# Kernel optimization log

Measured on AMD Instinct MI355X. Metric: run time of the kernel, lower is better.

Reference implementation:

```python
import jax, jax.numpy as jnp
import numpy as np

N, E, B = 100000, 3200000, 512
D_IN, D_H, HID = 500, 64, 200
NUM_CLASSES = 80
EPS_BN = 1e-5


def _sage(x, src, dst, Wl, bl, Wr):
    # PyG SAGEConv (mean aggr): out = lin_l(mean_{j->i} x_j) + lin_r(x_i)
    n = x.shape[0]
    agg = jax.ops.segment_sum(x[src], dst, num_segments=n)          # [n, d_in]
    deg = jax.ops.segment_sum(jnp.ones((src.shape[0],), x.dtype), dst, num_segments=n)
    mean = agg / jnp.maximum(deg, 1.0)[:, None]
    return mean @ Wl + bl + x @ Wr


def _bn(c, g, b):
    # BatchNorm1d, training-mode batch statistics (biased var)
    mu = c.mean(0)
    var = c.var(0)
    return (c - mu) / jnp.sqrt(var + EPS_BN) * g + b


def setup_inputs() -> dict:
    key = jax.random.key(0)
    ks = jax.random.split(key, 16)
    p = lambda k, shape: jax.random.normal(k, shape, dtype=jnp.float32) * 0.05
    z = lambda d: jnp.zeros((d,), jnp.float32)
    o = lambda d: jnp.ones((d,), jnp.float32)
    return {
        "x": jax.random.uniform(ks[0], (N, D_IN), dtype=jnp.float32),
        "edge_index": jax.random.randint(ks[1], (2, E), 0, N),
        "batch": jnp.sort(jax.random.randint(ks[2], (N,), 0, B)),
        "y": jax.random.randint(ks[3], (B,), 0, NUM_CLASSES),
        "conv1_Wl": p(ks[4], (D_IN, D_H)), "conv1_bl": z(D_H), "conv1_Wr": p(ks[5], (D_IN, D_H)),
        "conv2_Wl": p(ks[6], (D_H, D_H)),  "conv2_bl": z(D_H), "conv2_Wr": p(ks[7], (D_H, D_H)),
        "conv3_Wl": p(ks[8], (D_H, D_H)),  "conv3_bl": z(D_H), "conv3_Wr": p(ks[9], (D_H, D_H)),
        "lin1_W": p(ks[10], (D_H, HID)), "lin1_b": z(HID),
        "bn1_g": o(HID), "bn1_beta": z(HID),
        "lin2_W": p(ks[11], (HID, HID // 2)), "lin2_b": z(HID // 2),
        "bn2_g": o(HID // 2), "bn2_beta": z(HID // 2),
        "lin3_W": p(ks[12], (HID // 2, HID // 2)), "lin3_b": z(HID // 2),
        "bn3_g": o(HID // 2), "bn3_beta": z(HID // 2),
        "lin4_W": p(ks[13], (HID // 2, NUM_CLASSES)), "lin4_b": z(NUM_CLASSES),
    }


def reference(x, edge_index, batch, y,
              conv1_Wl, conv1_bl, conv1_Wr,
              conv2_Wl, conv2_bl, conv2_Wr,
              conv3_Wl, conv3_bl, conv3_Wr,
              lin1_W, lin1_b, bn1_g, bn1_beta,
              lin2_W, lin2_b, bn2_g, bn2_beta,
              lin3_W, lin3_b, bn3_g, bn3_beta,
              lin4_W, lin4_b):
    src, dst = edge_index[0], edge_index[1]
    # F.normalize(x, p=1.0, dim=-1)
    xn = x / jnp.maximum(jnp.abs(x).sum(-1, keepdims=True), 1e-12)
    e = _sage(xn, src, dst, conv1_Wl, conv1_bl, conv1_Wr)
    e = _sage(e, src, dst, conv2_Wl, conv2_bl, conv2_Wr)
    e = _sage(e, src, dst, conv3_Wl, conv3_bl, conv3_Wr)
    # global_mean_pool over graph ids
    sums = jax.ops.segment_sum(e, batch, num_segments=B)             # [B, 64]
    cnts = jax.ops.segment_sum(jnp.ones((e.shape[0],), e.dtype), batch, num_segments=B)
    c = sums / jnp.maximum(cnts, 1.0)[:, None]
    # dropout (p=0.1) omitted for a deterministic reference
    c = c @ lin1_W + lin1_b
    b = jnp.tanh(_bn(c, bn1_g, bn1_beta))
    c = b @ lin2_W + lin2_b
    b = jnp.tanh(_bn(c, bn2_g, bn2_beta))
    c = b @ lin3_W + lin3_b
    b = jnp.tanh(_bn(c, bn3_g, bn3_beta))
    return b @ lin4_W + lin4_b                                       # [B, 80]
```

## Files before the change

kernel.cpp:

```cpp
#include <hip/hip_runtime.h>
#include <hip/hip_bf16.h>

#define NN 100000
#define NE 3200000
#define NB 512
#define DIN 500
#define DH 64
#define HIDN 200
#define NCLS 80

#define NBUK 256
#define NPB 391
#define EPB 16384
#define NBLK_E ((NE + EPB - 1) / EPB)

typedef __attribute__((ext_vector_type(8))) short bf16x8;
typedef __attribute__((ext_vector_type(4))) float f32x4;

__device__ __forceinline__ short f2bf(float f) {
    union { float f; unsigned u; } v; v.f = f;
    unsigned r = v.u + 0x7FFF + ((v.u >> 16) & 1);
    return (short)(r >> 16);
}
__device__ __forceinline__ float bf2f(short s) {
    union { unsigned u; float f; } v; v.u = ((unsigned)(unsigned short)s) << 16;
    return v.f;
}

__global__ void bukhist_kernel(const int* __restrict__ dst, int* __restrict__ block_hist) {
    __shared__ int h[NBUK];
    for (int i = threadIdx.x; i < NBUK; i += 256) h[i] = 0;
    __syncthreads();
    int base = blockIdx.x * EPB;
    int end = min(base + EPB, NE);
    for (int e = base + threadIdx.x; e < end; e += 256)
        atomicAdd(&h[dst[e] / NPB], 1);
    __syncthreads();
    for (int i = threadIdx.x; i < NBUK; i += 256)
        block_hist[blockIdx.x * NBUK + i] = h[i];
}

__global__ void bukoff_kernel(int* __restrict__ block_hist, int* __restrict__ buk_base) {
    __shared__ int tot[NBUK];
    __shared__ int sc[NBUK];
    int b = threadIdx.x;
    int s = 0;
    for (int i = 0; i < NBLK_E; ++i) s += block_hist[i * NBUK + b];
    tot[b] = s; sc[b] = s;
    __syncthreads();
    for (int o = 1; o < NBUK; o <<= 1) {
        int t = (b >= o) ? sc[b - o] : 0;
        __syncthreads();
        sc[b] += t;
        __syncthreads();
    }
    int excl = sc[b] - tot[b];
    buk_base[b] = excl;
    if (b == NBUK - 1) buk_base[NBUK] = excl + tot[b];
    int run = excl;
    for (int i = 0; i < NBLK_E; ++i) {
        int idx = i * NBUK + b;
        int v = block_hist[idx];
        block_hist[idx] = run;
        run += v;
    }
}

__global__ void bukscat_kernel(const int* __restrict__ src, const int* __restrict__ dst,
                               const int* __restrict__ block_hist, int* __restrict__ bpack) {
    __shared__ int cur[NBUK];
    for (int i = threadIdx.x; i < NBUK; i += 256)
        cur[i] = block_hist[blockIdx.x * NBUK + i];
    __syncthreads();
    int base = blockIdx.x * EPB;
    int end = min(base + EPB, NE);
    for (int e = base + threadIdx.x; e < end; e += 256) {
        int d = dst[e];
        int bk = d / NPB;
        int p = atomicAdd(&cur[bk], 1);
        bpack[p] = (src[e] << 9) | (d - bk * NPB);
    }
}

__global__ void bukfin_kernel(const int* __restrict__ buk_base, const int* __restrict__ bpack,
                              int* __restrict__ row_ptr, float* __restrict__ invdeg,
                              int* __restrict__ csr_src) {
    __shared__ int cnt[NPB];
    __shared__ int cbase[NPB];
    int bk = blockIdx.x;
    int n0 = bk * NPB;
    int nloc = min(n0 + NPB, NN) - n0;
    for (int i = threadIdx.x; i < nloc; i += 256) cnt[i] = 0;
    __syncthreads();
    int beg = buk_base[bk], end = buk_base[bk + 1];
    for (int p = beg + threadIdx.x; p < end; p += 256)
        atomicAdd(&cnt[bpack[p] & 511], 1);
    __syncthreads();
    if (threadIdx.x == 0) {
        int run = beg;
        for (int i = 0; i < nloc; ++i) { int v = cnt[i]; cbase[i] = run; run += v; }
    }
    __syncthreads();
    for (int i = threadIdx.x; i < nloc; i += 256) {
        row_ptr[n0 + i] = cbase[i];
        invdeg[n0 + i] = 1.0f / fmaxf((float)cnt[i], 1.0f);
        cnt[i] = cbase[i];
    }
    if (bk == NBUK - 1 && threadIdx.x == 0) row_ptr[NN] = end;
    __syncthreads();
    for (int p = beg + threadIdx.x; p < end; p += 256) {
        int v = bpack[p];
        int q = atomicAdd(&cnt[v & 511], 1);
        csr_src[q] = v >> 9;
    }
}

__global__ void wprep_kernel(const float* __restrict__ Wl, const float* __restrict__ Wr,
                             short* __restrict__ Wb, int K, int KP) {
    int id = blockIdx.x * blockDim.x + threadIdx.x;
    if (id >= 128 * KP) return;
    int col = id / KP, k = id - col * KP;
    float v = 0.f;
    if (k < K) v = (col < 64) ? Wl[(size_t)k * 64 + col] : Wr[(size_t)k * 64 + (col - 64)];
    Wb[(size_t)col * KP + k] = f2bf(v);
}

__launch_bounds__(256)
__global__ void gemm_direct(const float* __restrict__ in, const short* __restrict__ Wb,
                            short* __restrict__ Hl, float* __restrict__ Hr) {
    const int tid = threadIdx.x;
    const int w = tid >> 6, l = tid & 63;
    const int q = l >> 4, r16 = l & 15;
    const int tile0 = blockIdx.x * 64 + w * 16;
    const int arow_i = tile0 + r16;
    const bool ok = arow_i < NN;
    const float* arow = in + (size_t)(ok ? arow_i : 0) * DIN + q * 8;

    f32x4 acc[8];
#pragma unroll
    for (int c = 0; c < 8; ++c) acc[c] = (f32x4){0.f, 0.f, 0.f, 0.f};
    float pabs = 0.f;

#pragma unroll
    for (int t = 0; t < 16; ++t) {
        float v[8];
        if (t < 15) {
            const float4 f0 = *(const float4*)(arow + t * 32);
            const float4 f1 = *(const float4*)(arow + t * 32 + 4);
            v[0] = f0.x; v[1] = f0.y; v[2] = f0.z; v[3] = f0.w;
            v[4] = f1.x; v[5] = f1.y; v[6] = f1.z; v[7] = f1.w;
        } else {
#pragma unroll
            for (int i = 0; i < 8; ++i) {
                int gk = t * 32 + q * 8 + i;
                v[i] = (gk < DIN) ? arow[t * 32 + i] : 0.f;
            }
        }
        short sh[8];
#pragma unroll
        for (int i = 0; i < 8; ++i) { pabs += fabsf(v[i]); sh[i] = f2bf(v[i]); }
        bf16x8 a = *(bf16x8*)sh;
#pragma unroll
        for (int c = 0; c < 8; ++c) {
            bf16x8 b = *(const bf16x8*)(Wb + (size_t)(c * 16 + r16) * 512 + t * 32 + q * 8);
            acc[c] = __builtin_amdgcn_mfma_f32_16x16x32_bf16(a, b, acc[c], 0, 0, 0);
        }
    }

    pabs += __shfl_xor(pabs, 16, 64);
    pabs += __shfl_xor(pabs, 32, 64);
    float sval = 1.0f / fmaxf(pabs, 1e-12f);

#pragma unroll
    for (int rr = 0; rr < 4; ++rr) {
        int lrow = q * 4 + rr;
        float srow = __shfl(sval, lrow, 64);
        int grow = tile0 + lrow;
        if (grow < NN) {
#pragma unroll
            for (int c = 0; c < 8; ++c) {
                float o = acc[c][rr] * srow;
                if (c < 4) Hl[(size_t)grow * 64 + c * 16 + r16] = f2bf(o);
                else       Hr[(size_t)grow * 64 + (c - 4) * 16 + r16] = o;
            }
        }
    }
}

__launch_bounds__(256)
__global__ void gemm64_mfma(const short* __restrict__ ein, const short* __restrict__ Wb,
                            short* __restrict__ Hl, float* __restrict__ Hr) {
    const int tid = threadIdx.x;
    const int row0 = blockIdx.x * 64;
    const int w = tid >> 6, l = tid & 63;
    const int q = l >> 4, r16 = l & 15;
    const int arow = row0 + w * 16 + r16;
    const bool ok = arow < NN;
    const short* ap = ein + (size_t)(ok ? arow : 0) * 64 + q * 8;
    f32x4 acc[8];
#pragma unroll
    for (int c = 0; c < 8; ++c) acc[c] = (f32x4){0.f, 0.f, 0.f, 0.f};
    const bf16x8 z8 = (bf16x8){0, 0, 0, 0, 0, 0, 0, 0};
#pragma unroll
    for (int t = 0; t < 2; ++t) {
        bf16x8 a = ok ? *(const bf16x8*)(ap + t * 32) : z8;
#pragma unroll
        for (int c = 0; c < 8; ++c) {
            bf16x8 b = *(const bf16x8*)(Wb + (size_t)(c * 16 + r16) * 64 + t * 32 + q * 8);
            acc[c] = __builtin_amdgcn_mfma_f32_16x16x32_bf16(a, b, acc[c], 0, 0, 0);
        }
    }
#pragma unroll
    for (int c = 0; c < 8; ++c) {
#pragma unroll
        for (int rr = 0; rr < 4; ++rr) {
            int grow = row0 + w * 16 + q * 4 + rr;
            if (grow < NN) {
                if (c < 4) Hl[(size_t)grow * 64 + c * 16 + r16] = f2bf(acc[c][rr]);
                else       Hr[(size_t)grow * 64 + (c - 4) * 16 + r16] = acc[c][rr];
            }
        }
    }
}

template<bool LAST>
__launch_bounds__(256, 8)
__global__ void gather_kernel(const int* __restrict__ row_ptr, const int* __restrict__ csr_src,
                              const short* __restrict__ Hl, const float* __restrict__ Hr,
                              const float* __restrict__ invdeg, const float* __restrict__ bl,
                              short* __restrict__ ebf, float* __restrict__ ef32) {
    int node = blockIdx.x * 4 + (threadIdx.x >> 6);
    if (node >= NN) return;
    int lane = threadIdx.x & 63;
    int ng = lane >> 3;
    int fl = lane & 7;
    int beg = row_ptr[node], end = row_ptr[node + 1];
    float a0[8], a1[8];
#pragma unroll
    for (int j = 0; j < 8; ++j) { a0[j] = 0.f; a1[j] = 0.f; }
    int p = beg + ng;
    for (; p + 24 < end; p += 32) {
        int s0 = csr_src[p];
        int s1 = csr_src[p + 8];
        int s2 = csr_src[p + 16];
        int s3 = csr_src[p + 24];
        bf16x8 v0 = *(const bf16x8*)(Hl + (size_t)s0 * 64 + fl * 8);
        bf16x8 v1 = *(const bf16x8*)(Hl + (size_t)s1 * 64 + fl * 8);
        bf16x8 v2 = *(const bf16x8*)(Hl + (size_t)s2 * 64 + fl * 8);
        bf16x8 v3 = *(const bf16x8*)(Hl + (size_t)s3 * 64 + fl * 8);
#pragma unroll
        for (int j = 0; j < 8; ++j) {
            a0[j] += bf2f(v0[j]) + bf2f(v2[j]);
            a1[j] += bf2f(v1[j]) + bf2f(v3[j]);
        }
    }
    for (; p < end; p += 8) {
        int s0 = csr_src[p];
        bf16x8 v0 = *(const bf16x8*)(Hl + (size_t)s0 * 64 + fl * 8);
#pragma unroll
        for (int j = 0; j < 8; ++j) a0[j] += bf2f(v0[j]);
    }
#pragma unroll
    for (int j = 0; j < 8; ++j) a0[j] += a1[j];
#pragma unroll
    for (int m = 8; m < 64; m <<= 1)
#pragma unroll
        for (int j = 0; j < 8; ++j) a0[j] += __shfl_xor(a0[j], m, 64);
    if (ng == 0) {
        float idg = invdeg[node];
        const float4 h0 = *(const float4*)(Hr + (size_t)node * 64 + fl * 8);
        const float4 h1 = *(const float4*)(Hr + (size_t)node * 64 + fl * 8 + 4);
        float o[8];
        o[0] = a0[0] * idg + bl[fl * 8 + 0] + h0.x;
        o[1] = a0[1] * idg + bl[fl * 8 + 1] + h0.y;
        o[2] = a0[2] * idg + bl[fl * 8 + 2] + h0.z;
        o[3] = a0[3] * idg + bl[fl * 8 + 3] + h0.w;
        o[4] = a0[4] * idg + bl[fl * 8 + 4] + h1.x;
        o[5] = a0[5] * idg + bl[fl * 8 + 5] + h1.y;
        o[6] = a0[6] * idg + bl[fl * 8 + 6] + h1.z;
        o[7] = a0[7] * idg + bl[fl * 8 + 7] + h1.w;
        if (LAST) {
            *(float4*)(ef32 + (size_t)node * 64 + fl * 8)     = make_float4(o[0], o[1], o[2], o[3]);
            *(float4*)(ef32 + (size_t)node * 64 + fl * 8 + 4) = make_float4(o[4], o[5], o[6], o[7]);
        } else {
            short s[8];
#pragma unroll
            for (int j = 0; j < 8; ++j) s[j] = f2bf(o[j]);
            *(bf16x8*)(ebf + (size_t)node * 64 + fl * 8) = *(bf16x8*)s;
        }
    }
}

__global__ void gseg_kernel(const int* __restrict__ batch, int* __restrict__ gstart) {
    int i = blockIdx.x * blockDim.x + threadIdx.x;
    if (i >= NN) return;
    int bc = batch[i];
    int bp = (i == 0) ? -1 : batch[i - 1];
    for (int b = bp + 1; b <= bc; ++b) gstart[b] = i;
    if (i == NN - 1)
        for (int b = bc + 1; b <= NB; ++b) gstart[b] = NN;
}

__launch_bounds__(256)
__global__ void pool_seg(const float* __restrict__ e, const int* __restrict__ gstart,
                         float* __restrict__ c0) {
    __shared__ float part[4][64];
    int b = blockIdx.x;
    int w = threadIdx.x >> 6, lane = threadIdx.x & 63;
    int s = gstart[b], t = gstart[b + 1];
    float acc = 0.f;
    for (int i = s + w; i < t; i += 4) acc += e[(size_t)i * 64 + lane];
    part[w][lane] = acc;
    __syncthreads();
    if (w == 0) {
        float v = part[0][lane] + part[1][lane] + part[2][lane] + part[3][lane];
        c0[b * 64 + lane] = v / fmaxf((float)(t - s), 1.0f);
    }
}

__global__ void lin_kernel(const float* __restrict__ in, const float* __restrict__ W,
                           const float* __restrict__ bias, float* __restrict__ out,
                           int Kd, int Dout) {
    int id = blockIdx.x * blockDim.x + threadIdx.x;
    if (id >= NB * Dout) return;
    int row = id / Dout, col = id - row * Dout;
    const float* ir = in + (size_t)row * Kd;
    float acc = bias[col];
    for (int k = 0; k < Kd; ++k) acc += ir[k] * W[(size_t)k * Dout + col];
    out[id] = acc;
}

__global__ void bnstats_kernel(const float* __restrict__ c, const float* __restrict__ g,
                               const float* __restrict__ beta, float* __restrict__ sa,
                               float* __restrict__ sb, int Dout) {
    int col = blockIdx.x;
    int tid = threadIdx.x;
    float s = 0.f, sq = 0.f;
    for (int r = tid; r < NB; r += 256) {
        float v = c[(size_t)r * Dout + col];
        s += v; sq += v * v;
    }
    __shared__ float ls[256], lq[256];
    ls[tid] = s; lq[tid] = sq;
    __syncthreads();
    for (int o = 128; o > 0; o >>= 1) {
        if (tid < o) { ls[tid] += ls[tid + o]; lq[tid] += lq[tid + o]; }
        __syncthreads();
    }
    if (tid == 0) {
        float mu = ls[0] / NB;
        float var = lq[0] / NB - mu * mu;
        float a = g[col] * rsqrtf(var + 1e-5f);
        sa[col] = a;
        sb[col] = beta[col] - mu * a;
    }
}

__global__ void bnapply_kernel(const float* __restrict__ c, const float* __restrict__ sa,
                               const float* __restrict__ sb, float* __restrict__ bv, int Dout) {
    int id = blockIdx.x * blockDim.x + threadIdx.x;
    if (id >= NB * Dout) return;
    int col = id % Dout;
    bv[id] = tanhf(c[id] * sa[col] + sb[col]);
}

extern "C" void kernel_launch(void* const* d_in, const int* in_sizes, int n_in,
                              void* d_out, int out_size, void* d_ws, size_t ws_size,
                              hipStream_t stream) {
    const float* x    = (const float*)d_in[0];
    const int* ei     = (const int*)d_in[1];
    const int* src    = ei;
    const int* dst    = ei + NE;
    const int* batch  = (const int*)d_in[2];
    const float* c1Wl = (const float*)d_in[4];
    const float* c1bl = (const float*)d_in[5];
    const float* c1Wr = (const float*)d_in[6];
    const float* c2Wl = (const float*)d_in[7];
    const float* c2bl = (const float*)d_in[8];
    const float* c2Wr = (const float*)d_in[9];
    const float* c3Wl = (const float*)d_in[10];
    const float* c3bl = (const float*)d_in[11];
    const float* c3Wr = (const float*)d_in[12];
    const float* l1W  = (const float*)d_in[13]; const float* l1b = (const float*)d_in[14];
    const float* bn1g = (const float*)d_in[15]; const float* bn1b = (const float*)d_in[16];
    const float* l2W  = (const float*)d_in[17]; const float* l2b = (const float*)d_in[18];
    const float* bn2g = (const float*)d_in[19]; const float* bn2b = (const float*)d_in[20];
    const float* l3W  = (const float*)d_in[21]; const float* l3b = (const float*)d_in[22];
    const float* bn3g = (const float*)d_in[23]; const float* bn3b = (const float*)d_in[24];
    const float* l4W  = (const float*)d_in[25]; const float* l4b = (const float*)d_in[26];
    float* out = (float*)d_out;

    char* wsb = (char*)d_ws;
    short* Hl     = (short*)wsb; wsb += (size_t)NN * 64 * 2;
    float* Hr     = (float*)wsb; wsb += (size_t)NN * 64 * 4;
    short* e      = (short*)wsb; wsb += (size_t)NN * 64 * 2;
    float* e3     = (float*)wsb; wsb += (size_t)NN * 64 * 4;
    float* invdeg = (float*)wsb; wsb += (size_t)NN * 4;
    float* c      = (float*)wsb; wsb += (size_t)NB * HIDN * 4;
    float* bv     = (float*)wsb; wsb += (size_t)NB * HIDN * 4;
    float* sa     = (float*)wsb; wsb += HIDN * 4;
    float* sb     = (float*)wsb; wsb += HIDN * 4;
    short* Wb1    = (short*)wsb; wsb += 128 * 512 * 2;
    short* Wb2    = (short*)wsb; wsb += 128 * 64 * 2;
    short* Wb3    = (short*)wsb; wsb += 128 * 64 * 2;
    int* row_ptr  = (int*)wsb;   wsb += (size_t)(NN + 1) * 4;
    int* csr_src  = (int*)wsb;   wsb += (size_t)NE * 4;
    int* buk_base = (int*)wsb;   wsb += (NBUK + 1) * 4;
    int* gstart   = (int*)wsb;   wsb += (NB + 1) * 4;
    int* bpack      = (int*)Hl;
    int* block_hist = (int*)e;

    bukhist_kernel<<<NBLK_E, 256, 0, stream>>>(dst, block_hist);
    bukoff_kernel<<<1, NBUK, 0, stream>>>(block_hist, buk_base);
    bukscat_kernel<<<NBLK_E, 256, 0, stream>>>(src, dst, block_hist, bpack);
    bukfin_kernel<<<NBUK, 256, 0, stream>>>(buk_base, bpack, row_ptr, invdeg, csr_src);

    gseg_kernel<<<(NN + 255) / 256, 256, 0, stream>>>(batch, gstart);

    wprep_kernel<<<(128 * 512 + 255) / 256, 256, 0, stream>>>(c1Wl, c1Wr, Wb1, DIN, 512);
    wprep_kernel<<<(128 * 64 + 255) / 256, 256, 0, stream>>>(c2Wl, c2Wr, Wb2, DH, 64);
    wprep_kernel<<<(128 * 64 + 255) / 256, 256, 0, stream>>>(c3Wl, c3Wr, Wb3, DH, 64);

    const int GB64 = (NN + 63) / 64;
    const int GGB  = (NN + 3) / 4;

    gemm_direct<<<GB64, 256, 0, stream>>>(x, Wb1, Hl, Hr);
    gather_kernel<false><<<GGB, 256, 0, stream>>>(row_ptr, csr_src, Hl, Hr, invdeg, c1bl, e, e3);
    gemm64_mfma<<<GB64, 256, 0, stream>>>(e, Wb2, Hl, Hr);
    gather_kernel<false><<<GGB, 256, 0, stream>>>(row_ptr, csr_src, Hl, Hr, invdeg, c2bl, e, e3);
    gemm64_mfma<<<GB64, 256, 0, stream>>>(e, Wb3, Hl, Hr);
    gather_kernel<true><<<GGB, 256, 0, stream>>>(row_ptr, csr_src, Hl, Hr, invdeg, c3bl, e, e3);

    pool_seg<<<NB, 256, 0, stream>>>(e3, gstart, bv);

    lin_kernel<<<(NB * 200 + 255) / 256, 256, 0, stream>>>(bv, l1W, l1b, c, 64, 200);
    bnstats_kernel<<<200, 256, 0, stream>>>(c, bn1g, bn1b, sa, sb, 200);
    bnapply_kernel<<<(NB * 200 + 255) / 256, 256, 0, stream>>>(c, sa, sb, bv, 200);

    lin_kernel<<<(NB * 100 + 255) / 256, 256, 0, stream>>>(bv, l2W, l2b, c, 200, 100);
    bnstats_kernel<<<100, 256, 0, stream>>>(c, bn2g, bn2b, sa, sb, 100);
    bnapply_kernel<<<(NB * 100 + 255) / 256, 256, 0, stream>>>(c, sa, sb, bv, 100);

    lin_kernel<<<(NB * 100 + 255) / 256, 256, 0, stream>>>(bv, l3W, l3b, c, 100, 100);
    bnstats_kernel<<<100, 256, 0, stream>>>(c, bn3g, bn3b, sa, sb, 100);
    bnapply_kernel<<<(NB * 100 + 255) / 256, 256, 0, stream>>>(c, sa, sb, bv, 100);

    lin_kernel<<<(NB * 80 + 255) / 256, 256, 0, stream>>>(bv, l4W, l4b, out, 100, 80);
}
```

Baseline: 652.0 us.

## Double-buffer layer-1 GEMM weights in LDS and shrink gather unroll

The first-layer GEMM now stages each 32-wide K slice of the bf16 weights into a double-buffered LDS tile, with the whole block loading cooperatively. Register prefetch of the A rows runs two steps ahead. Previously every wave read the weights directly from global memory. The gather kernel drops its minimum-occupancy launch bound and unrolls two edges per step instead of four, trading memory-level parallelism for lower register pressure. The GEMM adds barriers on every K step, and the gather keeps fewer loads in flight.

```diff
diff --git a/kernel.cpp b/kernel.cpp
--- a/kernel.cpp
+++ b/kernel.cpp
@@ -126,8 +126,9 @@
 }
 
 __launch_bounds__(256)
-__global__ void gemm_direct(const float* __restrict__ in, const short* __restrict__ Wb,
-                            short* __restrict__ Hl, float* __restrict__ Hr) {
+__global__ void gemm_hyb(const float* __restrict__ in, const short* __restrict__ Wb,
+                         short* __restrict__ Hl, float* __restrict__ Hr) {
+    __shared__ short B_lds[2][128][40];
     const int tid = threadIdx.x;
     const int w = tid >> 6, l = tid & 63;
     const int q = l >> 4, r16 = l & 15;
@@ -135,37 +136,97 @@
     const int arow_i = tile0 + r16;
     const bool ok = arow_i < NN;
     const float* arow = in + (size_t)(ok ? arow_i : 0) * DIN + q * 8;
+    const int sb_col = tid >> 1;
+    const int sb_kh  = (tid & 1) * 16;
+    const short* bsrc = Wb + (size_t)sb_col * 512 + sb_kh;
 
     f32x4 acc[8];
 #pragma unroll
     for (int c = 0; c < 8; ++c) acc[c] = (f32x4){0.f, 0.f, 0.f, 0.f};
     float pabs = 0.f;
-
-#pragma unroll
-    for (int t = 0; t < 16; ++t) {
-        float v[8];
-        if (t < 15) {
-            const float4 f0 = *(const float4*)(arow + t * 32);
-            const float4 f1 = *(const float4*)(arow + t * 32 + 4);
-            v[0] = f0.x; v[1] = f0.y; v[2] = f0.z; v[3] = f0.w;
-            v[4] = f1.x; v[5] = f1.y; v[6] = f1.z; v[7] = f1.w;
-        } else {
-#pragma unroll
-            for (int i = 0; i < 8; ++i) {
-                int gk = t * 32 + q * 8 + i;
-                v[i] = (gk < DIN) ? arow[t * 32 + i] : 0.f;
-            }
+    float va0[8], va1[8];
+    bf16x8 vb00, vb01, vb10, vb11;
+
+#define ISSUE(T, S) do { \
+    if ((T) < 15) { \
+        const float4 f0 = *(const float4*)(arow + (T) * 32); \
+        const float4 f1 = *(const float4*)(arow + (T) * 32 + 4); \
+        va##S[0] = f0.x; va##S[1] = f0.y; va##S[2] = f0.z; va##S[3] = f0.w; \
+        va##S[4] = f1.x; va##S[5] = f1.y; va##S[6] = f1.z; va##S[7] = f1.w; \
+    } else { \
+        _Pragma("unroll") \
+        for (int i = 0; i < 8; ++i) { \
+            int gk = (T) * 32 + q * 8 + i; \
+            va##S[i] = (gk < DIN) ? arow[(T) * 32 + i] : 0.f; \
+        } \
+    } \
+    vb##S##0 = *(const bf16x8*)(bsrc + (T) * 32); \
+    vb##S##1 = *(const bf16x8*)(bsrc + (T) * 32 + 8); \
+} while (0)
+
+#define STAGE_B(BUF, S) do { \
+    *(bf16x8*)&B_lds[BUF][sb_col][sb_kh]     = vb##S##0; \
+    *(bf16x8*)&B_lds[BUF][sb_col][sb_kh + 8] = vb##S##1; \
+} while (0)
+
+#define STEP(T, S) do { \
+    short sh[8]; \
+    _Pragma("unroll") \
+    for (int i = 0; i < 8; ++i) { pabs += fabsf(va##S[i]); sh[i] = f2bf(va##S[i]); } \
+    bf16x8 a = *(bf16x8*)sh; \
+    if ((T) + 2 < 16) ISSUE((T) + 2, S); \
+    _Pragma("unroll") \
+    for (int c = 0; c < 8; ++c) { \
+        bf16x8 b = *(bf16x8*)&B_lds[(T) & 1][c * 16 + r16][q * 8]; \
+        acc[c] = __builtin_amdgcn_mfma_f32_16x16x32_bf16(a, b, acc[c], 0, 0, 0); \
+    } \
+    if ((T) + 1 < 16) { \
+        STAGE_B(((T) + 1) & 1, S##_NEXT); \
+        __syncthreads(); \
+    } \
+} while (0)
+
+    ISSUE(0, 0); ISSUE(1, 1);
+    STAGE_B(0, 0);
+    __syncthreads();
+#define S0_NEXT 1
+#define S1_NEXT 0
+#pragma unroll
+    for (int tt = 0; tt < 8; ++tt) {
+        { short sh[8];
+#pragma unroll
+          for (int i = 0; i < 8; ++i) { pabs += fabsf(va0[i]); sh[i] = f2bf(va0[i]); }
+          bf16x8 a = *(bf16x8*)sh;
+          if (tt * 2 + 2 < 16) ISSUE(tt * 2 + 2, 0);
+#pragma unroll
+          for (int c = 0; c < 8; ++c) {
+              bf16x8 b = *(bf16x8*)&B_lds[0][c * 16 + r16][q * 8];
+              acc[c] = __builtin_amdgcn_mfma_f32_16x16x32_bf16(a, b, acc[c], 0, 0, 0);
+          }
+          STAGE_B(1, 1);
+          __syncthreads();
         }
-        short sh[8];
-#pragma unroll
-        for (int i = 0; i < 8; ++i) { pabs += fabsf(v[i]); sh[i] = f2bf(v[i]); }
-        bf16x8 a = *(bf16x8*)sh;
-#pragma unroll
-        for (int c = 0; c < 8; ++c) {
-            bf16x8 b = *(const bf16x8*)(Wb + (size_t)(c * 16 + r16) * 512 + t * 32 + q * 8);
-            acc[c] = __builtin_amdgcn_mfma_f32_16x16x32_bf16(a, b, acc[c], 0, 0, 0);
+        { short sh[8];
+#pragma unroll
+          for (int i = 0; i < 8; ++i) { pabs += fabsf(va1[i]); sh[i] = f2bf(va1[i]); }
+          bf16x8 a = *(bf16x8*)sh;
+          if (tt * 2 + 3 < 16) ISSUE(tt * 2 + 3, 1);
+#pragma unroll
+          for (int c = 0; c < 8; ++c) {
+              bf16x8 b = *(bf16x8*)&B_lds[1][c * 16 + r16][q * 8];
+              acc[c] = __builtin_amdgcn_mfma_f32_16x16x32_bf16(a, b, acc[c], 0, 0, 0);
+          }
+          if (tt < 7) {
+              STAGE_B(0, 0);
+              __syncthreads();
+          }
         }
     }
+#undef ISSUE
+#undef STAGE_B
+#undef STEP
+#undef S0_NEXT
+#undef S1_NEXT
 
     pabs += __shfl_xor(pabs, 16, 64);
     pabs += __shfl_xor(pabs, 32, 64);
@@ -224,7 +285,7 @@
 }
 
 template<bool LAST>
-__launch_bounds__(256, 8)
+__launch_bounds__(256)
 __global__ void gather_kernel(const int* __restrict__ row_ptr, const int* __restrict__ csr_src,
                               const short* __restrict__ Hl, const float* __restrict__ Hr,
                               const float* __restrict__ invdeg, const float* __restrict__ bl,
@@ -239,22 +300,15 @@
 #pragma unroll
     for (int j = 0; j < 8; ++j) { a0[j] = 0.f; a1[j] = 0.f; }
     int p = beg + ng;
-    for (; p + 24 < end; p += 32) {
+    for (; p + 8 < end; p += 16) {
         int s0 = csr_src[p];
         int s1 = csr_src[p + 8];
-        int s2 = csr_src[p + 16];
-        int s3 = csr_src[p + 24];
         bf16x8 v0 = *(const bf16x8*)(Hl + (size_t)s0 * 64 + fl * 8);
         bf16x8 v1 = *(const bf16x8*)(Hl + (size_t)s1 * 64 + fl * 8);
-        bf16x8 v2 = *(const bf16x8*)(Hl + (size_t)s2 * 64 + fl * 8);
-        bf16x8 v3 = *(const bf16x8*)(Hl + (size_t)s3 * 64 + fl * 8);
-#pragma unroll
-        for (int j = 0; j < 8; ++j) {
-            a0[j] += bf2f(v0[j]) + bf2f(v2[j]);
-            a1[j] += bf2f(v1[j]) + bf2f(v3[j]);
-        }
-    }
-    for (; p < end; p += 8) {
+#pragma unroll
+        for (int j = 0; j < 8; ++j) { a0[j] += bf2f(v0[j]); a1[j] += bf2f(v1[j]); }
+    }
+    if (p < end) {
         int s0 = csr_src[p];
         bf16x8 v0 = *(const bf16x8*)(Hl + (size_t)s0 * 64 + fl * 8);
 #pragma unroll
@@ -424,7 +478,7 @@
     const int GB64 = (NN + 63) / 64;
     const int GGB  = (NN + 3) / 4;
 
-    gemm_direct<<<GB64, 256, 0, stream>>>(x, Wb1, Hl, Hr);
+    gemm_hyb<<<GB64, 256, 0, stream>>>(x, Wb1, Hl, Hr);
     gather_kernel<false><<<GGB, 256, 0, stream>>>(row_ptr, csr_src, Hl, Hr, invdeg, c1bl, e, e3);
     gemm64_mfma<<<GB64, 256, 0, stream>>>(e, Wb2, Hl, Hr);
     gather_kernel<false><<<GGB, 256, 0, stream>>>(row_ptr, csr_src, Hl, Hr, invdeg, c2bl, e, e3);
```

Measured after the change: 595.2 us. 8.7% less time.

## Aggregate before transform in SAGE layers 2-3 and pre-swizzle layer-1 weights

Applied to the files above, without the earlier changes.

For layers 2 and 3 the order is swapped. The 64-dim bf16 embeddings are mean-aggregated first, then a single dual GEMM applies Wl to the mean and Wr to the node features, adds the bias and writes the output in place. This removes the intermediate fp32 Hr write and read, and the 128-wide GEMM output, per layer. Layer-1 weights are pre-packed in MFMA fragment order so each lane's loads are contiguous, and that loop is unrolled by 2. The gather loops drop from 4-way to 2-way unrolling, which may expose less memory-level parallelism.

```diff
diff --git a/kernel.cpp b/kernel.cpp
--- a/kernel.cpp
+++ b/kernel.cpp
@@ -115,19 +115,36 @@
     }
 }
 
-__global__ void wprep_kernel(const float* __restrict__ Wl, const float* __restrict__ Wr,
-                             short* __restrict__ Wb, int K, int KP) {
+__global__ void wprep_frag(const float* __restrict__ Wl, const float* __restrict__ Wr,
+                           short* __restrict__ Wf) {
     int id = blockIdx.x * blockDim.x + threadIdx.x;
-    if (id >= 128 * KP) return;
-    int col = id / KP, k = id - col * KP;
-    float v = 0.f;
-    if (k < K) v = (col < 64) ? Wl[(size_t)k * 64 + col] : Wr[(size_t)k * 64 + (col - 64)];
-    Wb[(size_t)col * KP + k] = f2bf(v);
+    if (id >= 16 * 8 * 64) return;
+    int l = id & 63;
+    int c = (id >> 6) & 7;
+    int t = id >> 9;
+    int q = l >> 4, r16 = l & 15;
+    int col = c * 16 + r16;
+    short v[8];
+#pragma unroll
+    for (int i = 0; i < 8; ++i) {
+        int k = t * 32 + q * 8 + i;
+        float f = 0.f;
+        if (k < DIN) f = (col < 64) ? Wl[(size_t)k * 64 + col] : Wr[(size_t)k * 64 + (col - 64)];
+        v[i] = f2bf(f);
+    }
+    *(bf16x8*)(Wf + (size_t)id * 8) = *(bf16x8*)v;
+}
+
+__global__ void wprep64(const float* __restrict__ W, short* __restrict__ Wb) {
+    int id = blockIdx.x * blockDim.x + threadIdx.x;
+    if (id >= 64 * 64) return;
+    int col = id >> 6, k = id & 63;
+    Wb[col * 64 + k] = f2bf(W[(size_t)k * 64 + col]);
 }
 
 __launch_bounds__(256)
-__global__ void gemm_direct(const float* __restrict__ in, const short* __restrict__ Wb,
-                            short* __restrict__ Hl, float* __restrict__ Hr) {
+__global__ void gemm_direct2(const float* __restrict__ in, const short* __restrict__ Wf,
+                             short* __restrict__ Hl, float* __restrict__ Hr) {
     const int tid = threadIdx.x;
     const int w = tid >> 6, l = tid & 63;
     const int q = l >> 4, r16 = l & 15;
@@ -135,13 +152,14 @@
     const int arow_i = tile0 + r16;
     const bool ok = arow_i < NN;
     const float* arow = in + (size_t)(ok ? arow_i : 0) * DIN + q * 8;
+    const short* wf = Wf + (size_t)l * 8;
 
     f32x4 acc[8];
 #pragma unroll
     for (int c = 0; c < 8; ++c) acc[c] = (f32x4){0.f, 0.f, 0.f, 0.f};
     float pabs = 0.f;
 
-#pragma unroll
+#pragma unroll 2
     for (int t = 0; t < 16; ++t) {
         float v[8];
         if (t < 15) {
@@ -162,7 +180,7 @@
         bf16x8 a = *(bf16x8*)sh;
 #pragma unroll
         for (int c = 0; c < 8; ++c) {
-            bf16x8 b = *(const bf16x8*)(Wb + (size_t)(c * 16 + r16) * 512 + t * 32 + q * 8);
+            bf16x8 b = *(const bf16x8*)(wf + ((size_t)(t * 8 + c) << 9));
             acc[c] = __builtin_amdgcn_mfma_f32_16x16x32_bf16(a, b, acc[c], 0, 0, 0);
         }
     }
@@ -188,47 +206,10 @@
 }
 
 __launch_bounds__(256)
-__global__ void gemm64_mfma(const short* __restrict__ ein, const short* __restrict__ Wb,
-                            short* __restrict__ Hl, float* __restrict__ Hr) {
-    const int tid = threadIdx.x;
-    const int row0 = blockIdx.x * 64;
-    const int w = tid >> 6, l = tid & 63;
-    const int q = l >> 4, r16 = l & 15;
-    const int arow = row0 + w * 16 + r16;
-    const bool ok = arow < NN;
-    const short* ap = ein + (size_t)(ok ? arow : 0) * 64 + q * 8;
-    f32x4 acc[8];
-#pragma unroll
-    for (int c = 0; c < 8; ++c) acc[c] = (f32x4){0.f, 0.f, 0.f, 0.f};
-    const bf16x8 z8 = (bf16x8){0, 0, 0, 0, 0, 0, 0, 0};
-#pragma unroll
-    for (int t = 0; t < 2; ++t) {
-        bf16x8 a = ok ? *(const bf16x8*)(ap + t * 32) : z8;
-#pragma unroll
-        for (int c = 0; c < 8; ++c) {
-            bf16x8 b = *(const bf16x8*)(Wb + (size_t)(c * 16 + r16) * 64 + t * 32 + q * 8);
-            acc[c] = __builtin_amdgcn_mfma_f32_16x16x32_bf16(a, b, acc[c], 0, 0, 0);
-        }
-    }
-#pragma unroll
-    for (int c = 0; c < 8; ++c) {
-#pragma unroll
-        for (int rr = 0; rr < 4; ++rr) {
-            int grow = row0 + w * 16 + q * 4 + rr;
-            if (grow < NN) {
-                if (c < 4) Hl[(size_t)grow * 64 + c * 16 + r16] = f2bf(acc[c][rr]);
-                else       Hr[(size_t)grow * 64 + (c - 4) * 16 + r16] = acc[c][rr];
-            }
-        }
-    }
-}
-
-template<bool LAST>
-__launch_bounds__(256, 8)
 __global__ void gather_kernel(const int* __restrict__ row_ptr, const int* __restrict__ csr_src,
                               const short* __restrict__ Hl, const float* __restrict__ Hr,
                               const float* __restrict__ invdeg, const float* __restrict__ bl,
-                              short* __restrict__ ebf, float* __restrict__ ef32) {
+                              short* __restrict__ ebf) {
     int node = blockIdx.x * 4 + (threadIdx.x >> 6);
     if (node >= NN) return;
     int lane = threadIdx.x & 63;
@@ -239,22 +220,15 @@
 #pragma unroll
     for (int j = 0; j < 8; ++j) { a0[j] = 0.f; a1[j] = 0.f; }
     int p = beg + ng;
-    for (; p + 24 < end; p += 32) {
+    for (; p + 8 < end; p += 16) {
         int s0 = csr_src[p];
         int s1 = csr_src[p + 8];
-        int s2 = csr_src[p + 16];
-        int s3 = csr_src[p + 24];
         bf16x8 v0 = *(const bf16x8*)(Hl + (size_t)s0 * 64 + fl * 8);
         bf16x8 v1 = *(const bf16x8*)(Hl + (size_t)s1 * 64 + fl * 8);
-        bf16x8 v2 = *(const bf16x8*)(Hl + (size_t)s2 * 64 + fl * 8);
-        bf16x8 v3 = *(const bf16x8*)(Hl + (size_t)s3 * 64 + fl * 8);
-#pragma unroll
-        for (int j = 0; j < 8; ++j) {
-            a0[j] += bf2f(v0[j]) + bf2f(v2[j]);
-            a1[j] += bf2f(v1[j]) + bf2f(v3[j]);
-        }
-    }
-    for (; p < end; p += 8) {
+#pragma unroll
+        for (int j = 0; j < 8; ++j) { a0[j] += bf2f(v0[j]); a1[j] += bf2f(v1[j]); }
+    }
+    if (p < end) {
         int s0 = csr_src[p];
         bf16x8 v0 = *(const bf16x8*)(Hl + (size_t)s0 * 64 + fl * 8);
 #pragma unroll
@@ -270,23 +244,103 @@
         float idg = invdeg[node];
         const float4 h0 = *(const float4*)(Hr + (size_t)node * 64 + fl * 8);
         const float4 h1 = *(const float4*)(Hr + (size_t)node * 64 + fl * 8 + 4);
-        float o[8];
-        o[0] = a0[0] * idg + bl[fl * 8 + 0] + h0.x;
-        o[1] = a0[1] * idg + bl[fl * 8 + 1] + h0.y;
-        o[2] = a0[2] * idg + bl[fl * 8 + 2] + h0.z;
-        o[3] = a0[3] * idg + bl[fl * 8 + 3] + h0.w;
-        o[4] = a0[4] * idg + bl[fl * 8 + 4] + h1.x;
-        o[5] = a0[5] * idg + bl[fl * 8 + 5] + h1.y;
-        o[6] = a0[6] * idg + bl[fl * 8 + 6] + h1.z;
-        o[7] = a0[7] * idg + bl[fl * 8 + 7] + h1.w;
-        if (LAST) {
-            *(float4*)(ef32 + (size_t)node * 64 + fl * 8)     = make_float4(o[0], o[1], o[2], o[3]);
-            *(float4*)(ef32 + (size_t)node * 64 + fl * 8 + 4) = make_float4(o[4], o[5], o[6], o[7]);
-        } else {
-            short s[8];
-#pragma unroll
-            for (int j = 0; j < 8; ++j) s[j] = f2bf(o[j]);
-            *(bf16x8*)(ebf + (size_t)node * 64 + fl * 8) = *(bf16x8*)s;
+        short s[8];
+        s[0] = f2bf(a0[0] * idg + bl[fl * 8 + 0] + h0.x);
+        s[1] = f2bf(a0[1] * idg + bl[fl * 8 + 1] + h0.y);
+        s[2] = f2bf(a0[2] * idg + bl[fl * 8 + 2] + h0.z);
+        s[3] = f2bf(a0[3] * idg + bl[fl * 8 + 3] + h0.w);
+        s[4] = f2bf(a0[4] * idg + bl[fl * 8 + 4] + h1.x);
+        s[5] = f2bf(a0[5] * idg + bl[fl * 8 + 5] + h1.y);
+        s[6] = f2bf(a0[6] * idg + bl[fl * 8 + 6] + h1.z);
+        s[7] = f2bf(a0[7] * idg + bl[fl * 8 + 7] + h1.w);
+        *(bf16x8*)(ebf + (size_t)node * 64 + fl * 8) = *(bf16x8*)s;
+    }
+}
+
+__launch_bounds__(256)
+__global__ void gathermean_kernel(const int* __restrict__ row_ptr, const int* __restrict__ csr_src,
+                                  const short* __restrict__ ein, const float* __restrict__ invdeg,
+                                  short* __restrict__ m) {
+    int node = blockIdx.x * 4 + (threadIdx.x >> 6);
+    if (node >= NN) return;
+    int lane = threadIdx.x & 63;
+    int ng = lane >> 3;
+    int fl = lane & 7;
+    int beg = row_ptr[node], end = row_ptr[node + 1];
+    float a0[8], a1[8];
+#pragma unroll
+    for (int j = 0; j < 8; ++j) { a0[j] = 0.f; a1[j] = 0.f; }
+    int p = beg + ng;
+    for (; p + 8 < end; p += 16) {
+        int s0 = csr_src[p];
+        int s1 = csr_src[p + 8];
+        bf16x8 v0 = *(const bf16x8*)(ein + (size_t)s0 * 64 + fl * 8);
+        bf16x8 v1 = *(const bf16x8*)(ein + (size_t)s1 * 64 + fl * 8);
+#pragma unroll
+        for (int j = 0; j < 8; ++j) { a0[j] += bf2f(v0[j]); a1[j] += bf2f(v1[j]); }
+    }
+    if (p < end) {
+        int s0 = csr_src[p];
+        bf16x8 v0 = *(const bf16x8*)(ein + (size_t)s0 * 64 + fl * 8);
+#pragma unroll
+        for (int j = 0; j < 8; ++j) a0[j] += bf2f(v0[j]);
+    }
+#pragma unroll
+    for (int j = 0; j < 8; ++j) a0[j] += a1[j];
+#pragma unroll
+    for (int mm = 8; mm < 64; mm <<= 1)
+#pragma unroll
+        for (int j = 0; j < 8; ++j) a0[j] += __shfl_xor(a0[j], mm, 64);
+    if (ng == 0) {
+        float idg = invdeg[node];
+        short s[8];
+#pragma unroll
+        for (int j = 0; j < 8; ++j) s[j] = f2bf(a0[j] * idg);
+        *(bf16x8*)(m + (size_t)node * 64 + fl * 8) = *(bf16x8*)s;
+    }
+}
+
+template<bool LAST>
+__launch_bounds__(256)
+__global__ void gemm_dual64(const short* __restrict__ m, const short* __restrict__ ein,
+                            const short* __restrict__ Wbl, const short* __restrict__ Wbr,
+                            const float* __restrict__ bl,
+                            short* __restrict__ eout, float* __restrict__ e3out) {
+    const int tid = threadIdx.x;
+    const int row0 = blockIdx.x * 64;
+    const int w = tid >> 6, l = tid & 63;
+    const int q = l >> 4, r16 = l & 15;
+    const int arow = row0 + w * 16 + r16;
+    const bool ok = arow < NN;
+    const short* mp = m   + (size_t)(ok ? arow : 0) * 64 + q * 8;
+    const short* ep = ein + (size_t)(ok ? arow : 0) * 64 + q * 8;
+    f32x4 acc[4];
+#pragma unroll
+    for (int c = 0; c < 4; ++c) acc[c] = (f32x4){0.f, 0.f, 0.f, 0.f};
+    const bf16x8 z8 = (bf16x8){0, 0, 0, 0, 0, 0, 0, 0};
+#pragma unroll
+    for (int t = 0; t < 2; ++t) {
+        bf16x8 am = ok ? *(const bf16x8*)(mp + t * 32) : z8;
+        bf16x8 ae = ok ? *(const bf16x8*)(ep + t * 32) : z8;
+#pragma unroll
+        for (int c = 0; c < 4; ++c) {
+            bf16x8 wl = *(const bf16x8*)(Wbl + (size_t)(c * 16 + r16) * 64 + t * 32 + q * 8);
+            bf16x8 wr = *(const bf16x8*)(Wbr + (size_t)(c * 16 + r16) * 64 + t * 32 + q * 8);
+            acc[c] = __builtin_amdgcn_mfma_f32_16x16x32_bf16(am, wl, acc[c], 0, 0, 0);
+            acc[c] = __builtin_amdgcn_mfma_f32_16x16x32_bf16(ae, wr, acc[c], 0, 0, 0);
+        }
+    }
+#pragma unroll
+    for (int c = 0; c < 4; ++c) {
+#pragma unroll
+        for (int rr = 0; rr < 4; ++rr) {
+            int grow = row0 + w * 16 + q * 4 + rr;
+            int col = c * 16 + r16;
+            if (grow < NN) {
+                float o = acc[c][rr] + bl[col];
+                if (LAST) e3out[(size_t)grow * 64 + col] = o;
+                else      eout[(size_t)grow * 64 + col]  = f2bf(o);
+            }
         }
     }
 }
@@ -394,15 +448,18 @@
     short* Hl     = (short*)wsb; wsb += (size_t)NN * 64 * 2;
     float* Hr     = (float*)wsb; wsb += (size_t)NN * 64 * 4;
     short* e      = (short*)wsb; wsb += (size_t)NN * 64 * 2;
+    short* m      = (short*)wsb; wsb += (size_t)NN * 64 * 2;
     float* e3     = (float*)wsb; wsb += (size_t)NN * 64 * 4;
     float* invdeg = (float*)wsb; wsb += (size_t)NN * 4;
     float* c      = (float*)wsb; wsb += (size_t)NB * HIDN * 4;
     float* bv     = (float*)wsb; wsb += (size_t)NB * HIDN * 4;
     float* sa     = (float*)wsb; wsb += HIDN * 4;
     float* sb     = (float*)wsb; wsb += HIDN * 4;
-    short* Wb1    = (short*)wsb; wsb += 128 * 512 * 2;
-    short* Wb2    = (short*)wsb; wsb += 128 * 64 * 2;
-    short* Wb3    = (short*)wsb; wsb += 128 * 64 * 2;
+    short* Wf1    = (short*)wsb; wsb += 16 * 8 * 64 * 8 * 2;
+    short* Wb2l   = (short*)wsb; wsb += 64 * 64 * 2;
+    short* Wb2r   = (short*)wsb; wsb += 64 * 64 * 2;
+    short* Wb3l   = (short*)wsb; wsb += 64 * 64 * 2;
+    short* Wb3r   = (short*)wsb; wsb += 64 * 64 * 2;
     int* row_ptr  = (int*)wsb;   wsb += (size_t)(NN + 1) * 4;
     int* csr_src  = (int*)wsb;   wsb += (size_t)NE * 4;
     int* buk_base = (int*)wsb;   wsb += (NBUK + 1) * 4;
@@ -417,19 +474,21 @@
 
     gseg_kernel<<<(NN + 255) / 256, 256, 0, stream>>>(batch, gstart);
 
-    wprep_kernel<<<(128 * 512 + 255) / 256, 256, 0, stream>>>(c1Wl, c1Wr, Wb1, DIN, 512);
-    wprep_kernel<<<(128 * 64 + 255) / 256, 256, 0, stream>>>(c2Wl, c2Wr, Wb2, DH, 64);
-    wprep_kernel<<<(128 * 64 + 255) / 256, 256, 0, stream>>>(c3Wl, c3Wr, Wb3, DH, 64);
+    wprep_frag<<<(16 * 8 * 64 + 255) / 256, 256, 0, stream>>>(c1Wl, c1Wr, Wf1);
+    wprep64<<<(64 * 64 + 255) / 256, 256, 0, stream>>>(c2Wl, Wb2l);
+    wprep64<<<(64 * 64 + 255) / 256, 256, 0, stream>>>(c2Wr, Wb2r);
+    wprep64<<<(64 * 64 + 255) / 256, 256, 0, stream>>>(c3Wl, Wb3l);
+    wprep64<<<(64 * 64 + 255) / 256, 256, 0, stream>>>(c3Wr, Wb3r);
 
     const int GB64 = (NN + 63) / 64;
     const int GGB  = (NN + 3) / 4;
 
-    gemm_direct<<<GB64, 256, 0, stream>>>(x, Wb1, Hl, Hr);
-    gather_kernel<false><<<GGB, 256, 0, stream>>>(row_ptr, csr_src, Hl, Hr, invdeg, c1bl, e, e3);
-    gemm64_mfma<<<GB64, 256, 0, stream>>>(e, Wb2, Hl, Hr);
-    gather_kernel<false><<<GGB, 256, 0, stream>>>(row_ptr, csr_src, Hl, Hr, invdeg, c2bl, e, e3);
-    gemm64_mfma<<<GB64, 256, 0, stream>>>(e, Wb3, Hl, Hr);
-    gather_kernel<true><<<GGB, 256, 0, stream>>>(row_ptr, csr_src, Hl, Hr, invdeg, c3bl, e, e3);
+    gemm_direct2<<<GB64, 256, 0, stream>>>(x, Wf1, Hl, Hr);
+    gather_kernel<<<GGB, 256, 0, stream>>>(row_ptr, csr_src, Hl, Hr, invdeg, c1bl, e);
+    gathermean_kernel<<<GGB, 256, 0, stream>>>(row_ptr, csr_src, e, invdeg, m);
+    gemm_dual64<false><<<GB64, 256, 0, stream>>>(m, e, Wb2l, Wb2r, c2bl, e, nullptr);
+    gathermean_kernel<<<GGB, 256, 0, stream>>>(row_ptr, csr_src, e, invdeg, m);
+    gemm_dual64<true><<<GB64, 256, 0, stream>>>(m, e, Wb3l, Wb3r, c3bl, nullptr, e3);
 
     pool_seg<<<NB, 256, 0, stream>>>(e3, gstart, bv);
 
```

After: 613.6 us. 1.06x faster.
